# Optimization experiments

Hardware: AMD Instinct MI355X
Metric: run time of the kernel (lower is better)

## Reference

```python
import jax, jax.numpy as jnp
import numpy as np

KV_H, Q_H, ATT_H = 256, 256, 128
B, S, SQ = 2, 1024, 512

def setup_inputs() -> dict:
    key = jax.random.key(0)
    ks = jax.random.split(key, 8)
    sc = lambda d: 1.0 / np.sqrt(d)
    return {
        "attention_kv": jax.random.normal(ks[0], (B, S, KV_H), dtype=jnp.float32),
        "attention_query": jax.random.normal(ks[1], (B, SQ, Q_H), dtype=jnp.float32),
        "W_kv": jax.random.uniform(ks[2], (KV_H, ATT_H), jnp.float32, -sc(KV_H), sc(KV_H)),
        "b_kv": jax.random.uniform(ks[3], (ATT_H,), jnp.float32, -sc(KV_H), sc(KV_H)),
        "W_q": jax.random.uniform(ks[4], (Q_H, ATT_H), jnp.float32, -sc(Q_H), sc(Q_H)),
        "b_q": jax.random.uniform(ks[5], (ATT_H,), jnp.float32, -sc(Q_H), sc(Q_H)),
        "w_v": jax.random.uniform(ks[6], (ATT_H,), jnp.float32, -sc(ATT_H), sc(ATT_H)),
        "b_v": jax.random.uniform(ks[7], (), jnp.float32, -sc(ATT_H), sc(ATT_H)),
    }

def reference(attention_kv, attention_query, W_kv, b_kv, W_q, b_q, w_v, b_v):
    # proj_kv: (B, S, A); proj_q: (B, Sq, A)
    proj_kv = jnp.einsum('bsh,ha->bsa', attention_kv, W_kv) + b_kv
    proj_q = jnp.einsum('bqh,ha->bqa', attention_query, W_q) + b_q
    # broadcast add + tanh -> (B, Sq, S, A)
    hidden = jnp.tanh(proj_kv[:, None, :, :] + proj_q[:, :, None, :])
    # scalar score per (b, q, s)
    attention_score = jnp.einsum('bqsa,a->bqs', hidden, w_v) + b_v
    attention_weight = jax.nn.softmax(attention_score, axis=-1)
    # weighted sum over kv sequence -> (B, Sq, KV_H)
    attention_output = jnp.einsum('bqs,bsh->bqh', attention_weight, attention_kv)
    return attention_output, attention_weight
```

## Files before the change

### kernel.cpp

```cpp
#include <hip/hip_runtime.h>
#include <hip/hip_bf16.h>

#define NB   2
#define SKV  1024
#define NSQ  512
#define HIN  256
#define HA   128

#define KSC   2.8853900817779268f
#define LOG2E 1.4426950408889634f

typedef float v2f __attribute__((ext_vector_type(2)));
__device__ __forceinline__ v2f pkfma(v2f a, v2f b, v2f c) {
    return __builtin_elementwise_fma(a, b, c);
}

__global__ __launch_bounds__(256) void proj_kernel(
    const float* __restrict__ kv,
    const float* __restrict__ qy,
    const float* __restrict__ Wkv,
    const float* __restrict__ bkv,
    const float* __restrict__ Wq,
    const float* __restrict__ bq,
    float* __restrict__ ek,
    float* __restrict__ eq)
{
    const int t  = threadIdx.x;
    const int c4 = (t & 31) * 4;
    const int r  = t >> 5;
    const int r0 = blockIdx.x * 8;
    const bool is_q = (r0 >= NB * SKV);
    const float* __restrict__ src = is_q ? (qy + (size_t)(r0 - NB * SKV) * HIN)
                                         : (kv + (size_t)r0 * HIN);
    const float* __restrict__ W  = is_q ? Wq : Wkv;
    const float* __restrict__ bs = is_q ? bq : bkv;
    float* __restrict__ dst = is_q ? (eq + (size_t)(r0 - NB * SKV) * HA)
                                   : (ek + (size_t)r0 * HA);

    const float* __restrict__ row = src + (size_t)r * HIN;
    v2f a0 = {0.f, 0.f}, a1 = {0.f, 0.f};
    #pragma unroll 4
    for (int h4 = 0; h4 < 64; ++h4) {
        const float4 x = *(const float4*)(row + h4 * 4);
        const float* Wb = W + (size_t)h4 * 4 * HA + c4;
        const float4 w0 = *(const float4*)(Wb);
        const float4 w1 = *(const float4*)(Wb + HA);
        const float4 w2 = *(const float4*)(Wb + 2 * HA);
        const float4 w3 = *(const float4*)(Wb + 3 * HA);
        a0 = pkfma((v2f){w0.x, w0.y}, (v2f){x.x, x.x}, a0);
        a1 = pkfma((v2f){w0.z, w0.w}, (v2f){x.x, x.x}, a1);
        a0 = pkfma((v2f){w1.x, w1.y}, (v2f){x.y, x.y}, a0);
        a1 = pkfma((v2f){w1.z, w1.w}, (v2f){x.y, x.y}, a1);
        a0 = pkfma((v2f){w2.x, w2.y}, (v2f){x.z, x.z}, a0);
        a1 = pkfma((v2f){w2.z, w2.w}, (v2f){x.z, x.z}, a1);
        a0 = pkfma((v2f){w3.x, w3.y}, (v2f){x.w, x.w}, a0);
        a1 = pkfma((v2f){w3.z, w3.w}, (v2f){x.w, x.w}, a1);
    }
    const float4 bb = *(const float4*)(bs + c4);
    float4 o;
    o.x = __builtin_amdgcn_exp2f((a0.x + bb.x) * KSC);
    o.y = __builtin_amdgcn_exp2f((a0.y + bb.y) * KSC);
    o.z = __builtin_amdgcn_exp2f((a1.x + bb.z) * KSC);
    o.w = __builtin_amdgcn_exp2f((a1.y + bb.w) * KSC);
    *(float4*)(dst + (size_t)r * HA + c4) = o;
}

__global__ __launch_bounds__(512) void score_kernel(
    const float* __restrict__ ek,
    const float* __restrict__ eq,
    const float* __restrict__ wv,
    const float* __restrict__ bv,
    float* __restrict__ ew,
    float* __restrict__ Dp)
{
    __shared__ __align__(16) float4 eqs[8][32];
    __shared__ __align__(16) float4 wvs[32];
    __shared__ float w0red[8];
    __shared__ float dred[8][8];

    const int t    = threadIdx.x;
    const int lane = t & 63, wid = t >> 6;
    const int blk  = blockIdx.x;
    const int sh   = blk & 1;
    const int oct  = blk >> 1;
    const int q0   = oct * 8;
    const int b    = q0 >> 9;
    const int s    = sh * 512 + t;

    if (t < 256) {
        const int j = t >> 5, f = t & 31;
        eqs[j][f] = *((const float4*)(eq + (size_t)(q0 + j) * HA) + f);
    } else if (t < 288) {
        wvs[t - 256] = ((const float4*)wv)[t - 256];
    }
    float w0p = wv[t & 127];
    #pragma unroll
    for (int o = 32; o > 0; o >>= 1) w0p += __shfl_down(w0p, o);
    if (lane == 0) w0red[wid] = w0p;
    const float bvf = bv[0];
    __syncthreads();
    const float W0 = w0red[0] + w0red[1];

    const float4* __restrict__ Erow4 = (const float4*)(ek + (size_t)(b * SKV + s) * HA);
    v2f acc[8];
    #pragma unroll
    for (int j = 0; j < 8; ++j) acc[j] = (v2f){0.f, 0.f};
    const v2f one = {1.f, 1.f};
    #pragma unroll 2
    for (int a4 = 0; a4 < 32; ++a4) {
        const float4 E  = Erow4[a4];
        const float4 w4 = wvs[a4];
        const v2f E01 = {E.x, E.y};
        const v2f E23 = {E.z, E.w};
        const v2f w01 = {w4.x, w4.y};
        const v2f w23 = {w4.z, w4.w};
        #pragma unroll
        for (int j = 0; j < 8; ++j) {
            const float4 qv = eqs[j][a4];
            const v2f A  = pkfma(E01, (v2f){qv.x, qv.y}, one);
            const v2f B  = pkfma(E23, (v2f){qv.z, qv.w}, one);
            const v2f m  = A * B;
            const float r = __builtin_amdgcn_rcpf(m.x * m.y);
            const v2f ts = (v2f){m.y, m.x} * (v2f){r, r};
            acc[j] = pkfma(w01, ts * B, acc[j]);
            acc[j] = pkfma(w23, ts * A, acc[j]);
        }
    }

    float ev[8];
    #pragma unroll
    for (int j = 0; j < 8; ++j) {
        const float score = fmaf(-2.f, acc[j].x + acc[j].y, W0) + bvf;
        ev[j] = __builtin_amdgcn_exp2f(score * LOG2E);
        ew[(size_t)(q0 + j) * SKV + s] = ev[j];
    }
    #pragma unroll
    for (int j = 0; j < 8; ++j) {
        float ss = ev[j];
        #pragma unroll
        for (int o = 32; o > 0; o >>= 1) ss += __shfl_down(ss, o);
        if (lane == 0) dred[wid][j] = ss;
    }
    __syncthreads();
    if (t < 8) {
        float d = 0.f;
        #pragma unroll
        for (int w = 0; w < 8; ++w) d += dred[w][t];
        Dp[(size_t)sh * 1024 + q0 + t] = d;
    }
}

__global__ __launch_bounds__(512) void out_kernel(
    const float* __restrict__ ew,
    const float* __restrict__ Dp,
    const float* __restrict__ kv,
    float* __restrict__ out)
{
    __shared__ __align__(16) float lds[SKV * 12];
    __shared__ float rws[8];

    const int t    = threadIdx.x;
    const int lane = t & 63, wid = t >> 6;
    const int blk  = blockIdx.x;
    const int hh   = blk & 1;
    const int oct  = blk >> 1;
    const int q0   = oct * 8;
    const int b    = q0 >> 9;

    if (t < 8) rws[t] = 1.0f / (Dp[q0 + t] + Dp[1024 + q0 + t]);
    __syncthreads();
    float rw[8];
    #pragma unroll
    for (int j = 0; j < 8; ++j) rw[j] = rws[j];

    float* __restrict__ outw = out + (size_t)NB * NSQ * HIN;
    #pragma unroll
    for (int p = 0; p < 2; ++p) {
        const int s = wid * 128 + p * 64 + lane;
        float e[8];
        #pragma unroll
        for (int j = 0; j < 8; ++j) e[j] = ew[(size_t)(q0 + j) * SKV + s] * rw[j];
        if (hh == 0) {
            #pragma unroll
            for (int j = 0; j < 8; ++j) outw[(size_t)(q0 + j) * SKV + s] = e[j];
        }
        float* d = lds + (size_t)s * 12;
        *(float4*)(d)     = make_float4(e[0], e[1], e[2], e[3]);
        *(float4*)(d + 4) = make_float4(e[4], e[5], e[6], e[7]);
    }
    __syncthreads();

    const int hq  = t & 31;
    const int sc0 = t >> 5;
    const int h   = hh * 128 + hq * 4;
    const float* __restrict__ kvb = kv + (size_t)b * SKV * HIN + h;
    v2f acc[8][2];
    #pragma unroll
    for (int j = 0; j < 8; ++j) { acc[j][0] = (v2f){0.f, 0.f}; acc[j][1] = (v2f){0.f, 0.f}; }
    #pragma unroll 4
    for (int i = 0; i < 64; ++i) {
        const int s = sc0 * 64 + i;
        const float4 v = *(const float4*)(kvb + (size_t)s * HIN);
        const float* er = lds + (size_t)s * 12;
        const float4 e03 = *(const float4*)(er);
        const float4 e47 = *(const float4*)(er + 4);
        const v2f vlo = {v.x, v.y}, vhi = {v.z, v.w};
        acc[0][0] = pkfma(vlo, (v2f){e03.x, e03.x}, acc[0][0]);
        acc[0][1] = pkfma(vhi, (v2f){e03.x, e03.x}, acc[0][1]);
        acc[1][0] = pkfma(vlo, (v2f){e03.y, e03.y}, acc[1][0]);
        acc[1][1] = pkfma(vhi, (v2f){e03.y, e03.y}, acc[1][1]);
        acc[2][0] = pkfma(vlo, (v2f){e03.z, e03.z}, acc[2][0]);
        acc[2][1] = pkfma(vhi, (v2f){e03.z, e03.z}, acc[2][1]);
        acc[3][0] = pkfma(vlo, (v2f){e03.w, e03.w}, acc[3][0]);
        acc[3][1] = pkfma(vhi, (v2f){e03.w, e03.w}, acc[3][1]);
        acc[4][0] = pkfma(vlo, (v2f){e47.x, e47.x}, acc[4][0]);
        acc[4][1] = pkfma(vhi, (v2f){e47.x, e47.x}, acc[4][1]);
        acc[5][0] = pkfma(vlo, (v2f){e47.y, e47.y}, acc[5][0]);
        acc[5][1] = pkfma(vhi, (v2f){e47.y, e47.y}, acc[5][1]);
        acc[6][0] = pkfma(vlo, (v2f){e47.z, e47.z}, acc[6][0]);
        acc[6][1] = pkfma(vhi, (v2f){e47.z, e47.z}, acc[6][1]);
        acc[7][0] = pkfma(vlo, (v2f){e47.w, e47.w}, acc[7][0]);
        acc[7][1] = pkfma(vhi, (v2f){e47.w, e47.w}, acc[7][1]);
    }

    #pragma unroll
    for (int j = 0; j < 8; ++j) {
        #pragma unroll
        for (int k = 0; k < 2; ++k) {
            acc[j][k].x += __shfl_down(acc[j][k].x, 32);
            acc[j][k].y += __shfl_down(acc[j][k].y, 32);
        }
    }
    __syncthreads();
    if (lane < 32) {
        float* pp = lds + (size_t)wid * 1024 + hq * 4;
        #pragma unroll
        for (int j = 0; j < 8; ++j)
            *(float4*)(pp + (size_t)j * 128) =
                make_float4(acc[j][0].x, acc[j][0].y, acc[j][1].x, acc[j][1].y);
    }
    __syncthreads();
    #pragma unroll
    for (int k = 0; k < 2; ++k) {
        const int id = t + k * 512;
        const int j = id >> 7, hl = id & 127;
        float v = 0.f;
        #pragma unroll
        for (int g = 0; g < 8; ++g) v += lds[(size_t)g * 1024 + j * 128 + hl];
        out[(size_t)(q0 + j) * HIN + hh * 128 + hl] = v;
    }
}

extern "C" void kernel_launch(void* const* d_in, const int* in_sizes, int n_in,
                              void* d_out, int out_size, void* d_ws, size_t ws_size,
                              hipStream_t stream) {
    (void)in_sizes; (void)n_in; (void)out_size; (void)ws_size;
    const float* kv  = (const float*)d_in[0];
    const float* qy  = (const float*)d_in[1];
    const float* Wkv = (const float*)d_in[2];
    const float* bkv = (const float*)d_in[3];
    const float* Wq  = (const float*)d_in[4];
    const float* bq  = (const float*)d_in[5];
    const float* wv  = (const float*)d_in[6];
    const float* bv  = (const float*)d_in[7];

    float* ek = (float*)d_ws;
    float* eq = ek + 262144;
    float* ew = eq + 131072;
    float* Dp = ew + 1048576;
    float* out = (float*)d_out;

    hipLaunchKernelGGL(proj_kernel, dim3(384), dim3(256), 0, stream,
                       kv, qy, Wkv, bkv, Wq, bq, ek, eq);
    hipLaunchKernelGGL(score_kernel, dim3(256), dim3(512), 0, stream,
                       ek, eq, wv, bv, ew, Dp);
    hipLaunchKernelGGL(out_kernel, dim3(256), dim3(512), 0, stream,
                       ew, Dp, kv, out);
}
```

Baseline: 124.6 us.

## Transpose kv projection, drop softmax constants, split-K output with partial reduction kernel

Result: slower. 129.4 us (+3.8%).

```diff
diff --git a/kernel.cpp b/kernel.cpp
--- a/kernel.cpp
+++ b/kernel.cpp
@@ -1,14 +1,14 @@
 #include <hip/hip_runtime.h>
-#include <hip/hip_bf16.h>
 
 #define NB   2
 #define SKV  1024
 #define NSQ  512
 #define HIN  256
 #define HA   128
-
-#define KSC   2.8853900817779268f
-#define LOG2E 1.4426950408889634f
+#define NQ   (NB * NSQ)
+#define NR   (NB * SKV)
+
+#define KSC 2.8853900817779268f
 
 typedef float v2f __attribute__((ext_vector_type(2)));
 __device__ __forceinline__ v2f pkfma(v2f a, v2f b, v2f c) {
@@ -16,110 +16,90 @@
 }
 
 __global__ __launch_bounds__(256) void proj_kernel(
-    const float* __restrict__ kv,
-    const float* __restrict__ qy,
-    const float* __restrict__ Wkv,
-    const float* __restrict__ bkv,
-    const float* __restrict__ Wq,
-    const float* __restrict__ bq,
-    float* __restrict__ ek,
+    const float* __restrict__ kv,  const float* __restrict__ qy,
+    const float* __restrict__ Wkv, const float* __restrict__ bkv,
+    const float* __restrict__ Wq,  const float* __restrict__ bq,
+    float* __restrict__ ekT,
     float* __restrict__ eq)
 {
-    const int t  = threadIdx.x;
-    const int c4 = (t & 31) * 4;
-    const int r  = t >> 5;
-    const int r0 = blockIdx.x * 8;
-    const bool is_q = (r0 >= NB * SKV);
-    const float* __restrict__ src = is_q ? (qy + (size_t)(r0 - NB * SKV) * HIN)
-                                         : (kv + (size_t)r0 * HIN);
+    const int t = threadIdx.x;
+    const int a = t & 127;
+    const int g = __builtin_amdgcn_readfirstlane(t >> 7);
+    const int blk = blockIdx.x;
+    const bool is_q = blk >= 256;
+    const int r0 = (is_q ? (blk - 256) : blk) * 8 + g * 4;
+    const float* __restrict__ src = (is_q ? qy : kv) + (size_t)r0 * HIN;
     const float* __restrict__ W  = is_q ? Wq : Wkv;
     const float* __restrict__ bs = is_q ? bq : bkv;
-    float* __restrict__ dst = is_q ? (eq + (size_t)(r0 - NB * SKV) * HA)
-                                   : (ek + (size_t)r0 * HA);
-
-    const float* __restrict__ row = src + (size_t)r * HIN;
-    v2f a0 = {0.f, 0.f}, a1 = {0.f, 0.f};
-    #pragma unroll 4
-    for (int h4 = 0; h4 < 64; ++h4) {
-        const float4 x = *(const float4*)(row + h4 * 4);
-        const float* Wb = W + (size_t)h4 * 4 * HA + c4;
-        const float4 w0 = *(const float4*)(Wb);
-        const float4 w1 = *(const float4*)(Wb + HA);
-        const float4 w2 = *(const float4*)(Wb + 2 * HA);
-        const float4 w3 = *(const float4*)(Wb + 3 * HA);
-        a0 = pkfma((v2f){w0.x, w0.y}, (v2f){x.x, x.x}, a0);
-        a1 = pkfma((v2f){w0.z, w0.w}, (v2f){x.x, x.x}, a1);
-        a0 = pkfma((v2f){w1.x, w1.y}, (v2f){x.y, x.y}, a0);
-        a1 = pkfma((v2f){w1.z, w1.w}, (v2f){x.y, x.y}, a1);
-        a0 = pkfma((v2f){w2.x, w2.y}, (v2f){x.z, x.z}, a0);
-        a1 = pkfma((v2f){w2.z, w2.w}, (v2f){x.z, x.z}, a1);
-        a0 = pkfma((v2f){w3.x, w3.y}, (v2f){x.w, x.w}, a0);
-        a1 = pkfma((v2f){w3.z, w3.w}, (v2f){x.w, x.w}, a1);
-    }
-    const float4 bb = *(const float4*)(bs + c4);
-    float4 o;
-    o.x = __builtin_amdgcn_exp2f((a0.x + bb.x) * KSC);
-    o.y = __builtin_amdgcn_exp2f((a0.y + bb.y) * KSC);
-    o.z = __builtin_amdgcn_exp2f((a1.x + bb.z) * KSC);
-    o.w = __builtin_amdgcn_exp2f((a1.y + bb.w) * KSC);
-    *(float4*)(dst + (size_t)r * HA + c4) = o;
-}
-
-__global__ __launch_bounds__(512) void score_kernel(
-    const float* __restrict__ ek,
+
+    float ac0 = 0.f, ac1 = 0.f, ac2 = 0.f, ac3 = 0.f;
+    #pragma unroll 8
+    for (int h = 0; h < HIN; ++h) {
+        const float w  = W[(size_t)h * HA + a];
+        const float x0 = src[h];
+        const float x1 = src[HIN + h];
+        const float x2 = src[2 * HIN + h];
+        const float x3 = src[3 * HIN + h];
+        ac0 = fmaf(x0, w, ac0);
+        ac1 = fmaf(x1, w, ac1);
+        ac2 = fmaf(x2, w, ac2);
+        ac3 = fmaf(x3, w, ac3);
+    }
+    const float bb = bs[a];
+    const float o0 = __builtin_amdgcn_exp2f((ac0 + bb) * KSC);
+    const float o1 = __builtin_amdgcn_exp2f((ac1 + bb) * KSC);
+    const float o2 = __builtin_amdgcn_exp2f((ac2 + bb) * KSC);
+    const float o3 = __builtin_amdgcn_exp2f((ac3 + bb) * KSC);
+    if (!is_q) {
+        float* __restrict__ d = ekT + (size_t)a * NR + r0;
+        d[0] = o0; d[1] = o1; d[2] = o2; d[3] = o3;
+    } else {
+        eq[(size_t)(r0 + 0) * HA + a] = o0;
+        eq[(size_t)(r0 + 1) * HA + a] = o1;
+        eq[(size_t)(r0 + 2) * HA + a] = o2;
+        eq[(size_t)(r0 + 3) * HA + a] = o3;
+    }
+}
+
+__global__ __launch_bounds__(256) void score_kernel(
+    const float* __restrict__ ekT,
     const float* __restrict__ eq,
     const float* __restrict__ wv,
-    const float* __restrict__ bv,
     float* __restrict__ ew,
+    float* __restrict__ ewT,
     float* __restrict__ Dp)
 {
-    __shared__ __align__(16) float4 eqs[8][32];
-    __shared__ __align__(16) float4 wvs[32];
-    __shared__ float w0red[8];
-    __shared__ float dred[8][8];
-
-    const int t    = threadIdx.x;
+    __shared__ float dred[4][8];
+    const int t = threadIdx.x;
     const int lane = t & 63, wid = t >> 6;
-    const int blk  = blockIdx.x;
-    const int sh   = blk & 1;
-    const int oct  = blk >> 1;
-    const int q0   = oct * 8;
-    const int b    = q0 >> 9;
-    const int s    = sh * 512 + t;
-
-    if (t < 256) {
-        const int j = t >> 5, f = t & 31;
-        eqs[j][f] = *((const float4*)(eq + (size_t)(q0 + j) * HA) + f);
-    } else if (t < 288) {
-        wvs[t - 256] = ((const float4*)wv)[t - 256];
-    }
-    float w0p = wv[t & 127];
-    #pragma unroll
-    for (int o = 32; o > 0; o >>= 1) w0p += __shfl_down(w0p, o);
-    if (lane == 0) w0red[wid] = w0p;
-    const float bvf = bv[0];
-    __syncthreads();
-    const float W0 = w0red[0] + w0red[1];
-
-    const float4* __restrict__ Erow4 = (const float4*)(ek + (size_t)(b * SKV + s) * HA);
+    const int blk = blockIdx.x;
+    const int sq  = blk & 3;
+    const int oct = blk >> 2;
+    const int q0  = oct * 8;
+    const int b   = q0 >> 9;
+    const int s   = sq * 256 + t;
+    const int srow = b * SKV + s;
+
     v2f acc[8];
     #pragma unroll
     for (int j = 0; j < 8; ++j) acc[j] = (v2f){0.f, 0.f};
     const v2f one = {1.f, 1.f};
+
     #pragma unroll 2
     for (int a4 = 0; a4 < 32; ++a4) {
-        const float4 E  = Erow4[a4];
-        const float4 w4 = wvs[a4];
-        const v2f E01 = {E.x, E.y};
-        const v2f E23 = {E.z, E.w};
-        const v2f w01 = {w4.x, w4.y};
-        const v2f w23 = {w4.z, w4.w};
+        const float E0 = ekT[(size_t)(a4 * 4 + 0) * NR + srow];
+        const float E1 = ekT[(size_t)(a4 * 4 + 1) * NR + srow];
+        const float E2 = ekT[(size_t)(a4 * 4 + 2) * NR + srow];
+        const float E3 = ekT[(size_t)(a4 * 4 + 3) * NR + srow];
+        const float4 w4 = *(const float4*)(wv + a4 * 4);
+        const v2f E01 = {E0, E1}, E23 = {E2, E3};
+        const v2f w01 = {w4.x, w4.y}, w23 = {w4.z, w4.w};
         #pragma unroll
         for (int j = 0; j < 8; ++j) {
-            const float4 qv = eqs[j][a4];
-            const v2f A  = pkfma(E01, (v2f){qv.x, qv.y}, one);
-            const v2f B  = pkfma(E23, (v2f){qv.z, qv.w}, one);
-            const v2f m  = A * B;
+            const float4 qv = *(const float4*)(eq + (size_t)(q0 + j) * HA + a4 * 4);
+            const v2f A = pkfma(E01, (v2f){qv.x, qv.y}, one);
+            const v2f B = pkfma(E23, (v2f){qv.z, qv.w}, one);
+            const v2f m = A * B;
             const float r = __builtin_amdgcn_rcpf(m.x * m.y);
             const v2f ts = (v2f){m.y, m.x} * (v2f){r, r};
             acc[j] = pkfma(w01, ts * B, acc[j]);
@@ -130,9 +110,13 @@
     float ev[8];
     #pragma unroll
     for (int j = 0; j < 8; ++j) {
-        const float score = fmaf(-2.f, acc[j].x + acc[j].y, W0) + bvf;
-        ev[j] = __builtin_amdgcn_exp2f(score * LOG2E);
+        ev[j] = __builtin_amdgcn_exp2f(-KSC * (acc[j].x + acc[j].y));
         ew[(size_t)(q0 + j) * SKV + s] = ev[j];
+    }
+    {
+        float* __restrict__ wp = ewT + ((size_t)oct * SKV + s) * 8;
+        *(float4*)(wp)     = make_float4(ev[0], ev[1], ev[2], ev[3]);
+        *(float4*)(wp + 4) = make_float4(ev[4], ev[5], ev[6], ev[7]);
     }
     #pragma unroll
     for (int j = 0; j < 8; ++j) {
@@ -143,112 +127,82 @@
     }
     __syncthreads();
     if (t < 8) {
-        float d = 0.f;
+        float d = dred[0][t] + dred[1][t] + dred[2][t] + dred[3][t];
+        Dp[(size_t)sq * NQ + q0 + t] = d;
+    }
+}
+
+__global__ __launch_bounds__(512) void out_kernel(
+    const float* __restrict__ ewT,
+    const float* __restrict__ kv,
+    float* __restrict__ P)
+{
+    const int t = threadIdx.x;
+    const int lane = t & 63;
+    const int wu = __builtin_amdgcn_readfirstlane(t >> 6);
+    const int blk = blockIdx.x;
+    const int k  = blk & 3;
+    const int gi = blk >> 2;
+    const int q0 = gi * 16;
+    const int b  = q0 >> 9;
+    const int o0 = q0 >> 3;
+
+    v2f acc[16][2];
+    #pragma unroll
+    for (int j = 0; j < 16; ++j) { acc[j][0] = (v2f){0.f, 0.f}; acc[j][1] = (v2f){0.f, 0.f}; }
+
+    const int sbase = k * 256 + wu * 32;
+    const float* __restrict__ kvb = kv + ((size_t)b * SKV + sbase) * HIN + lane * 4;
+    const float* __restrict__ wA = ewT + ((size_t)o0 * SKV + sbase) * 8;
+    const float* __restrict__ wB = ewT + ((size_t)(o0 + 1) * SKV + sbase) * 8;
+
+    #pragma unroll 4
+    for (int i = 0; i < 32; ++i) {
+        const float4 v = *(const float4*)(kvb + (size_t)i * HIN);
+        const v2f vlo = {v.x, v.y}, vhi = {v.z, v.w};
+        const float4 a0 = *(const float4*)(wA + (size_t)i * 8);
+        const float4 a1 = *(const float4*)(wA + (size_t)i * 8 + 4);
+        const float4 b0 = *(const float4*)(wB + (size_t)i * 8);
+        const float4 b1 = *(const float4*)(wB + (size_t)i * 8 + 4);
+        const float wq[16] = {a0.x, a0.y, a0.z, a0.w, a1.x, a1.y, a1.z, a1.w,
+                              b0.x, b0.y, b0.z, b0.w, b1.x, b1.y, b1.z, b1.w};
         #pragma unroll
-        for (int w = 0; w < 8; ++w) d += dred[w][t];
-        Dp[(size_t)sh * 1024 + q0 + t] = d;
-    }
-}
-
-__global__ __launch_bounds__(512) void out_kernel(
+        for (int j = 0; j < 16; ++j) {
+            const v2f wj = {wq[j], wq[j]};
+            acc[j][0] = pkfma(vlo, wj, acc[j][0]);
+            acc[j][1] = pkfma(vhi, wj, acc[j][1]);
+        }
+    }
+    float* __restrict__ Pp = P + (size_t)(k * 8 + wu) * ((size_t)NQ * HIN);
+    #pragma unroll
+    for (int j = 0; j < 16; ++j) {
+        *(float4*)(Pp + (size_t)(q0 + j) * HIN + lane * 4) =
+            make_float4(acc[j][0].x, acc[j][0].y, acc[j][1].x, acc[j][1].y);
+    }
+}
+
+__global__ __launch_bounds__(256) void final_kernel(
     const float* __restrict__ ew,
     const float* __restrict__ Dp,
-    const float* __restrict__ kv,
+    const float* __restrict__ P,
     float* __restrict__ out)
 {
-    __shared__ __align__(16) float lds[SKV * 12];
-    __shared__ float rws[8];
-
-    const int t    = threadIdx.x;
-    const int lane = t & 63, wid = t >> 6;
-    const int blk  = blockIdx.x;
-    const int hh   = blk & 1;
-    const int oct  = blk >> 1;
-    const int q0   = oct * 8;
-    const int b    = q0 >> 9;
-
-    if (t < 8) rws[t] = 1.0f / (Dp[q0 + t] + Dp[1024 + q0 + t]);
-    __syncthreads();
-    float rw[8];
-    #pragma unroll
-    for (int j = 0; j < 8; ++j) rw[j] = rws[j];
-
-    float* __restrict__ outw = out + (size_t)NB * NSQ * HIN;
-    #pragma unroll
-    for (int p = 0; p < 2; ++p) {
-        const int s = wid * 128 + p * 64 + lane;
-        float e[8];
-        #pragma unroll
-        for (int j = 0; j < 8; ++j) e[j] = ew[(size_t)(q0 + j) * SKV + s] * rw[j];
-        if (hh == 0) {
-            #pragma unroll
-            for (int j = 0; j < 8; ++j) outw[(size_t)(q0 + j) * SKV + s] = e[j];
-        }
-        float* d = lds + (size_t)s * 12;
-        *(float4*)(d)     = make_float4(e[0], e[1], e[2], e[3]);
-        *(float4*)(d + 4) = make_float4(e[4], e[5], e[6], e[7]);
-    }
-    __syncthreads();
-
-    const int hq  = t & 31;
-    const int sc0 = t >> 5;
-    const int h   = hh * 128 + hq * 4;
-    const float* __restrict__ kvb = kv + (size_t)b * SKV * HIN + h;
-    v2f acc[8][2];
-    #pragma unroll
-    for (int j = 0; j < 8; ++j) { acc[j][0] = (v2f){0.f, 0.f}; acc[j][1] = (v2f){0.f, 0.f}; }
-    #pragma unroll 4
-    for (int i = 0; i < 64; ++i) {
-        const int s = sc0 * 64 + i;
-        const float4 v = *(const float4*)(kvb + (size_t)s * HIN);
-        const float* er = lds + (size_t)s * 12;
-        const float4 e03 = *(const float4*)(er);
-        const float4 e47 = *(const float4*)(er + 4);
-        const v2f vlo = {v.x, v.y}, vhi = {v.z, v.w};
-        acc[0][0] = pkfma(vlo, (v2f){e03.x, e03.x}, acc[0][0]);
-        acc[0][1] = pkfma(vhi, (v2f){e03.x, e03.x}, acc[0][1]);
-        acc[1][0] = pkfma(vlo, (v2f){e03.y, e03.y}, acc[1][0]);
-        acc[1][1] = pkfma(vhi, (v2f){e03.y, e03.y}, acc[1][1]);
-        acc[2][0] = pkfma(vlo, (v2f){e03.z, e03.z}, acc[2][0]);
-        acc[2][1] = pkfma(vhi, (v2f){e03.z, e03.z}, acc[2][1]);
-        acc[3][0] = pkfma(vlo, (v2f){e03.w, e03.w}, acc[3][0]);
-        acc[3][1] = pkfma(vhi, (v2f){e03.w, e03.w}, acc[3][1]);
-        acc[4][0] = pkfma(vlo, (v2f){e47.x, e47.x}, acc[4][0]);
-        acc[4][1] = pkfma(vhi, (v2f){e47.x, e47.x}, acc[4][1]);
-        acc[5][0] = pkfma(vlo, (v2f){e47.y, e47.y}, acc[5][0]);
-        acc[5][1] = pkfma(vhi, (v2f){e47.y, e47.y}, acc[5][1]);
-        acc[6][0] = pkfma(vlo, (v2f){e47.z, e47.z}, acc[6][0]);
-        acc[6][1] = pkfma(vhi, (v2f){e47.z, e47.z}, acc[6][1]);
-        acc[7][0] = pkfma(vlo, (v2f){e47.w, e47.w}, acc[7][0]);
-        acc[7][1] = pkfma(vhi, (v2f){e47.w, e47.w}, acc[7][1]);
-    }
-
-    #pragma unroll
-    for (int j = 0; j < 8; ++j) {
-        #pragma unroll
-        for (int k = 0; k < 2; ++k) {
-            acc[j][k].x += __shfl_down(acc[j][k].x, 32);
-            acc[j][k].y += __shfl_down(acc[j][k].y, 32);
-        }
-    }
-    __syncthreads();
-    if (lane < 32) {
-        float* pp = lds + (size_t)wid * 1024 + hq * 4;
-        #pragma unroll
-        for (int j = 0; j < 8; ++j)
-            *(float4*)(pp + (size_t)j * 128) =
-                make_float4(acc[j][0].x, acc[j][0].y, acc[j][1].x, acc[j][1].y);
-    }
-    __syncthreads();
-    #pragma unroll
-    for (int k = 0; k < 2; ++k) {
-        const int id = t + k * 512;
-        const int j = id >> 7, hl = id & 127;
-        float v = 0.f;
-        #pragma unroll
-        for (int g = 0; g < 8; ++g) v += lds[(size_t)g * 1024 + j * 128 + hl];
-        out[(size_t)(q0 + j) * HIN + hh * 128 + hl] = v;
-    }
+    const int t = threadIdx.x;
+    const int q = blockIdx.x;
+    const float D = Dp[q] + Dp[NQ + q] + Dp[2 * NQ + q] + Dp[3 * NQ + q];
+    const float rw = 1.0f / D;
+
+    float* __restrict__ outw = out + (size_t)NQ * HIN;
+    #pragma unroll
+    for (int c = 0; c < 4; ++c) {
+        const int s = c * 256 + t;
+        outw[(size_t)q * SKV + s] = ew[(size_t)q * SKV + s] * rw;
+    }
+    float v = 0.f;
+    #pragma unroll
+    for (int p = 0; p < 32; ++p)
+        v += P[(size_t)p * ((size_t)NQ * HIN) + (size_t)q * HIN + t];
+    out[(size_t)q * HIN + t] = v * rw;
 }
 
 extern "C" void kernel_launch(void* const* d_in, const int* in_sizes, int n_in,
@@ -263,17 +217,22 @@
     const float* bq  = (const float*)d_in[5];
     const float* wv  = (const float*)d_in[6];
     const float* bv  = (const float*)d_in[7];
-
-    float* ek = (float*)d_ws;
-    float* eq = ek + 262144;
-    float* ew = eq + 131072;
-    float* Dp = ew + 1048576;
+    (void)bv;
+
+    float* ekT = (float*)d_ws;
+    float* eq  = ekT + 262144;
+    float* ew  = eq  + 131072;
+    float* ewT = ew  + 1048576;
+    float* Dp  = ewT + 1048576;
+    float* P   = Dp  + 4096;
     float* out = (float*)d_out;
 
-    hipLaunchKernelGGL(proj_kernel, dim3(384), dim3(256), 0, stream,
-                       kv, qy, Wkv, bkv, Wq, bq, ek, eq);
-    hipLaunchKernelGGL(score_kernel, dim3(256), dim3(512), 0, stream,
-                       ek, eq, wv, bv, ew, Dp);
-    hipLaunchKernelGGL(out_kernel, dim3(256), dim3(512), 0, stream,
-                       ew, Dp, kv, out);
-}
+    hipLaunchKernelGGL(proj_kernel,  dim3(384),  dim3(256), 0, stream,
+                       kv, qy, Wkv, bkv, Wq, bq, ekT, eq);
+    hipLaunchKernelGGL(score_kernel, dim3(512),  dim3(256), 0, stream,
+                       ekT, eq, wv, ew, ewT, Dp);
+    hipLaunchKernelGGL(out_kernel,   dim3(256),  dim3(512), 0, stream,
+                       ewT, kv, P);
+    hipLaunchKernelGGL(final_kernel, dim3(1024), dim3(256), 0, stream,
+                       ew, Dp, P, out);
+}
```
